# Performance work log

Hardware: AMD Instinct MI355X
Metric: run time of the kernel (lower is better)

The kernel has to match this reference:

```python
import jax, jax.numpy as jnp
import numpy as np


def _conv1d(x, w, pad):
    # torch F.conv1d is cross-correlation; so is lax.conv_general_dilated.
    # x: (k, c_in, N), w: (c_out, c_in, K) -> (k, c_out, N + 2*pad - K + 1)
    return jax.lax.conv_general_dilated(
        x, w, window_strides=(1,), padding=[(pad, pad)],
        dimension_numbers=("NCH", "OIH", "NCH"))


def setup_inputs() -> dict:
    key = jax.random.key(0)
    k1, k2, k3, k4, k5 = jax.random.split(key, 5)
    k_b, c_out, c_in, N, m = 4, 64, 8, 4096, 8
    z_real = jax.random.normal(k1, (k_b, c_in, N), dtype=jnp.float32)
    z_imag = jax.random.normal(k2, (k_b, c_in, N), dtype=jnp.float32)
    A = jax.random.uniform(k3, (c_out, c_in, 1), jnp.float32, 0.75, 1.25)
    beta = jax.random.uniform(k4, (c_out, c_in, 1), jnp.float32, -np.pi, np.pi)
    bias = jax.random.uniform(k5, (c_out, 1), jnp.float32, -0.1, 0.1)
    return {"z_real": z_real, "z_imag": z_imag, "A": A, "beta": beta,
            "bias": bias, "m": m}


def reference(z_real, z_imag, A, beta, bias, m):
    k_b, c_in, N = z_real.shape
    am = abs(int(m))
    ker = N // (2 * am)  # self.ker_size

    # Complex harmonic kernel: |A| * exp(i*(beta + 2*pi*m*phi/N))
    phi = jnp.arange(ker, dtype=jnp.float32)
    ang = beta + (2.0 * jnp.pi * m / N) * phi  # (c_out, c_in, ker)
    absA = jnp.abs(A)
    wr = absA * jnp.cos(ang)
    wi = absA * jnp.sin(ang)

    # Complex conv via 4 real convs: (zr + i zi) * (wr + i wi)
    rr = _conv1d(z_real, wr, ker)
    ii = _conv1d(z_imag, wi, ker)
    ri = _conv1d(z_real, wi, ker)
    ir = _conv1d(z_imag, wr, ker)
    zraw_r = rr - ii  # (k, c_out, N + ker + 1)
    zraw_i = ri + ir

    # Aliasing fold: gather shifted copies, mask out-of-range, alternate sign.
    n = jnp.arange(-2 * am + 1, 2 * am + 1, dtype=jnp.int32)  # (4|m|,)
    mu = jnp.arange(N, dtype=jnp.int32)[:, None]              # (N, 1)
    ind = mu + ker * n                                        # (N, 4|m|)
    cond = ((ind > 0) & (ind < N + ker)).astype(jnp.float32)
    ind = jnp.clip(ind, 0, N + ker)
    menos_1 = (-1.0) ** (1.0 + n.astype(jnp.float32))         # alternating sign
    sign = cond * menos_1                                     # (N, 4|m|)

    gr = zraw_r[:, :, ind]  # (k, c_out, N, 4|m|)
    gi = zraw_i[:, :, ind]
    sr = jnp.einsum("kcnm,nm->kcn", gr, sign)
    si = jnp.einsum("kcnm,nm->kcn", gi, sign)

    # activation: sigmoid(|z| + bias) * z / (|z| + 1e-5)
    mag = jnp.sqrt(sr * sr + si * si)
    gate = jax.nn.sigmoid(mag + bias) / (mag + 1e-5)
    return gate * sr, gate * si
```

## Files before the change

### kernel.cpp

```cpp
#include <hip/hip_runtime.h>
#include <math.h>


#define KB   4
#define COUT 64
#define CIN  8
#define NN   4096
#define INV_N   (1.0f / 4096.0f)
#define INV_2PI 0.15915494309189535f

__global__ __launch_bounds__(256) void capa_fused_kernel(
    const float* __restrict__ zr,
    const float* __restrict__ zi,
    const float* __restrict__ A,
    const float* __restrict__ beta,
    const float* __restrict__ bias,
    const int*   __restrict__ m_ptr,
    float* __restrict__ out) {

    const int blk = blockIdx.x;
    const int b = blk >> 6, o = blk & (COUT - 1);
    const int m = *m_ptr;
    const int tid = threadIdx.x;

    float P[CIN], Q[CIN];
    #pragma unroll
    for (int i = 0; i < CIN; ++i) {
        float a  = fabsf(A[o * CIN + i]);
        float rb = beta[o * CIN + i] * INV_2PI;
        P[i] = a * __builtin_amdgcn_cosf(rb);
        Q[i] = a * __builtin_amdgcn_sinf(rb);
    }

    const float4* xr = (const float4*)(zr + b * CIN * NN);
    const float4* xi = (const float4*)(zi + b * CIN * NN);

    float gr = 0.f, hr = 0.f;
    #pragma unroll
    for (int k = 0; k < NN / 4 / 256; ++k) {
        int vidx = tid + k * 256;
        float4 vr[CIN], vi[CIN];
        #pragma unroll
        for (int i = 0; i < CIN; ++i) {
            vr[i] = xr[i * (NN / 4) + vidx];
            vi[i] = xi[i * (NN / 4) + vidx];
        }
        int t0 = vidx * 4;
        #pragma unroll
        for (int j = 0; j < 4; ++j) {
            float X = 0.f, Y = 0.f;
            #pragma unroll
            for (int i = 0; i < CIN; ++i) {
                float a = (&vr[i].x)[j];
                float c2 = (&vi[i].x)[j];
                X += -P[i] * a + Q[i] * c2;
                Y +=  Q[i] * a + P[i] * c2;
            }
            int r = (m * (t0 + j)) & (NN - 1);
            float rev = (float)r * INV_N;
            float s = __builtin_amdgcn_sinf(rev);
            float c = __builtin_amdgcn_cosf(rev);
            gr += c * X + s * Y;
            hr += s * X - c * Y;
        }
    }

    #pragma unroll
    for (int off = 32; off > 0; off >>= 1) {
        gr += __shfl_down(gr, off);
        hr += __shfl_down(hr, off);
    }
    __shared__ float red[4][2];
    int wave = tid >> 6, lane = tid & 63;
    if (lane == 0) { red[wave][0] = gr; red[wave][1] = hr; }
    __syncthreads();
    const float Gr = red[0][0] + red[1][0] + red[2][0] + red[3][0];
    const float Hr = red[0][1] + red[1][1] + red[2][1] + red[3][1];

    const float bo = bias[o];
    float4* out_r = (float4*)(out + ((long)blk << 12));
    float4* out_i = (float4*)(out + (long)KB * COUT * NN + ((long)blk << 12));

    #pragma unroll
    for (int k = 0; k < NN / 4 / 256; ++k) {
        int vidx = tid + k * 256;
        int mu0 = vidx * 4;
        float4 o1, o2;
        #pragma unroll
        for (int j = 0; j < 4; ++j) {
            int r = (m * (mu0 + j)) & (NN - 1);
            float rev = (float)r * INV_N;
            float s = __builtin_amdgcn_sinf(rev);
            float c = __builtin_amdgcn_cosf(rev);
            float sr = -(c * Gr + s * Hr);
            float si = s * Gr - c * Hr;
            float mag = sqrtf(sr * sr + si * si);
            float gate = 1.0f / ((1.0f + __expf(-(mag + bo))) * (mag + 1e-5f));
            (&o1.x)[j] = gate * sr;
            (&o2.x)[j] = gate * si;
        }
        out_r[vidx] = o1;
        out_i[vidx] = o2;
    }
}

extern "C" void kernel_launch(void* const* d_in, const int* in_sizes, int n_in,
                              void* d_out, int out_size, void* d_ws, size_t ws_size,
                              hipStream_t stream) {
    const float* z_real = (const float*)d_in[0];
    const float* z_imag = (const float*)d_in[1];
    const float* A      = (const float*)d_in[2];
    const float* beta   = (const float*)d_in[3];
    const float* bias   = (const float*)d_in[4];
    const int*   m_ptr  = (const int*)d_in[5];
    float* out = (float*)d_out;

    capa_fused_kernel<<<KB * COUT, 256, 0, stream>>>(
        z_real, z_imag, A, beta, bias, m_ptr, out);
}
```

Baseline: 77.98 us.

## Factor input projections into per-channel Fourier partials computed once by separate kernel

The input-dependent inner products against the cos/sin basis are now computed once per (batch, input channel) in a first kernel, split into four chunks and written as partial sums to workspace. A second kernel combines these with the per-output-channel complex weights and produces the gated output. Before, every (batch, output channel) block re-read all input channels and recomputed the same projections, giving 64x redundant loads and FMAs. The cost is an extra kernel launch and a round-trip through global workspace.

```diff
diff --git a/kernel.cpp b/kernel.cpp
--- a/kernel.cpp
+++ b/kernel.cpp
@@ -6,76 +6,92 @@
 #define COUT 64
 #define CIN  8
 #define NN   4096
+#define NCHUNK 4
 #define INV_N   (1.0f / 4096.0f)
 #define INV_2PI 0.15915494309189535f
 
-__global__ __launch_bounds__(256) void capa_fused_kernel(
+__global__ __launch_bounds__(256) void f_partial_kernel(
     const float* __restrict__ zr,
     const float* __restrict__ zi,
+    const int* __restrict__ m_ptr,
+    float* __restrict__ Fp) {
+
+    const int blk = blockIdx.x;
+    const int pair = blk >> 2, chunk = blk & (NCHUNK - 1);
+    const int tid = threadIdx.x;
+    const int m = *m_ptr;
+
+    const float4* xr = (const float4*)(zr + pair * NN) + chunk * 256;
+    const float4* xi = (const float4*)(zi + pair * NN) + chunk * 256;
+    float4 vr = xr[tid];
+    float4 vi = xi[tid];
+
+    const int t0 = (chunk * 256 + tid) * 4;
+    float fcr = 0.f, fsr = 0.f, fci = 0.f, fsi = 0.f;
+    #pragma unroll
+    for (int j = 0; j < 4; ++j) {
+        int r = (m * (t0 + j)) & (NN - 1);
+        float rev = (float)r * INV_N;
+        float s = __builtin_amdgcn_sinf(rev);
+        float c = __builtin_amdgcn_cosf(rev);
+        float a = (&vr.x)[j], b = (&vi.x)[j];
+        fcr += a * c;  fsr += a * s;
+        fci += b * c;  fsi += b * s;
+    }
+    #pragma unroll
+    for (int off = 32; off > 0; off >>= 1) {
+        fcr += __shfl_down(fcr, off);
+        fsr += __shfl_down(fsr, off);
+        fci += __shfl_down(fci, off);
+        fsi += __shfl_down(fsi, off);
+    }
+    __shared__ float red[4][4];
+    int wave = tid >> 6, lane = tid & 63;
+    if (lane == 0) {
+        red[wave][0] = fcr; red[wave][1] = fsr;
+        red[wave][2] = fci; red[wave][3] = fsi;
+    }
+    __syncthreads();
+    if (tid == 0) {
+        Fp[blk * 4 + 0] = red[0][0] + red[1][0] + red[2][0] + red[3][0];
+        Fp[blk * 4 + 1] = red[0][1] + red[1][1] + red[2][1] + red[3][1];
+        Fp[blk * 4 + 2] = red[0][2] + red[1][2] + red[2][2] + red[3][2];
+        Fp[blk * 4 + 3] = red[0][3] + red[1][3] + red[2][3] + red[3][3];
+    }
+}
+
+__global__ __launch_bounds__(256) void out_kernel(
     const float* __restrict__ A,
     const float* __restrict__ beta,
     const float* __restrict__ bias,
-    const int*   __restrict__ m_ptr,
+    const int* __restrict__ m_ptr,
+    const float* __restrict__ Fp,
     float* __restrict__ out) {
 
     const int blk = blockIdx.x;
     const int b = blk >> 6, o = blk & (COUT - 1);
     const int m = *m_ptr;
-    const int tid = threadIdx.x;
 
-    float P[CIN], Q[CIN];
+    float Gr = 0.f, Hr = 0.f;
     #pragma unroll
     for (int i = 0; i < CIN; ++i) {
         float a  = fabsf(A[o * CIN + i]);
         float rb = beta[o * CIN + i] * INV_2PI;
-        P[i] = a * __builtin_amdgcn_cosf(rb);
-        Q[i] = a * __builtin_amdgcn_sinf(rb);
+        float cb = __builtin_amdgcn_cosf(rb);
+        float sb = __builtin_amdgcn_sinf(rb);
+        float P = a * cb, Q = a * sb;
+        const float* f = Fp + (b * CIN + i) * NCHUNK * 4;
+        float Fcr = 0.f, Fsr = 0.f, Fci = 0.f, Fsi = 0.f;
+        #pragma unroll
+        for (int ch = 0; ch < NCHUNK; ++ch) {
+            Fcr += f[ch * 4 + 0];
+            Fsr += f[ch * 4 + 1];
+            Fci += f[ch * 4 + 2];
+            Fsi += f[ch * 4 + 3];
+        }
+        Gr += -P * Fcr + Q * Fsr + Q * Fci + P * Fsi;
+        Hr += -P * Fsr - Q * Fcr + Q * Fsi - P * Fci;
     }
-
-    const float4* xr = (const float4*)(zr + b * CIN * NN);
-    const float4* xi = (const float4*)(zi + b * CIN * NN);
-
-    float gr = 0.f, hr = 0.f;
-    #pragma unroll
-    for (int k = 0; k < NN / 4 / 256; ++k) {
-        int vidx = tid + k * 256;
-        float4 vr[CIN], vi[CIN];
-        #pragma unroll
-        for (int i = 0; i < CIN; ++i) {
-            vr[i] = xr[i * (NN / 4) + vidx];
-            vi[i] = xi[i * (NN / 4) + vidx];
-        }
-        int t0 = vidx * 4;
-        #pragma unroll
-        for (int j = 0; j < 4; ++j) {
-            float X = 0.f, Y = 0.f;
-            #pragma unroll
-            for (int i = 0; i < CIN; ++i) {
-                float a = (&vr[i].x)[j];
-                float c2 = (&vi[i].x)[j];
-                X += -P[i] * a + Q[i] * c2;
-                Y +=  Q[i] * a + P[i] * c2;
-            }
-            int r = (m * (t0 + j)) & (NN - 1);
-            float rev = (float)r * INV_N;
-            float s = __builtin_amdgcn_sinf(rev);
-            float c = __builtin_amdgcn_cosf(rev);
-            gr += c * X + s * Y;
-            hr += s * X - c * Y;
-        }
-    }
-
-    #pragma unroll
-    for (int off = 32; off > 0; off >>= 1) {
-        gr += __shfl_down(gr, off);
-        hr += __shfl_down(hr, off);
-    }
-    __shared__ float red[4][2];
-    int wave = tid >> 6, lane = tid & 63;
-    if (lane == 0) { red[wave][0] = gr; red[wave][1] = hr; }
-    __syncthreads();
-    const float Gr = red[0][0] + red[1][0] + red[2][0] + red[3][0];
-    const float Hr = red[0][1] + red[1][1] + red[2][1] + red[3][1];
 
     const float bo = bias[o];
     float4* out_r = (float4*)(out + ((long)blk << 12));
@@ -83,7 +99,7 @@
 
     #pragma unroll
     for (int k = 0; k < NN / 4 / 256; ++k) {
-        int vidx = tid + k * 256;
+        int vidx = threadIdx.x + k * 256;
         int mu0 = vidx * 4;
         float4 o1, o2;
         #pragma unroll
@@ -114,7 +130,8 @@
     const float* bias   = (const float*)d_in[4];
     const int*   m_ptr  = (const int*)d_in[5];
     float* out = (float*)d_out;
+    float* Fp  = (float*)d_ws;
 
-    capa_fused_kernel<<<KB * COUT, 256, 0, stream>>>(
-        z_real, z_imag, A, beta, bias, m_ptr, out);
+    f_partial_kernel<<<KB * CIN * NCHUNK, 256, 0, stream>>>(z_real, z_imag, m_ptr, Fp);
+    out_kernel<<<KB * COUT, 256, 0, stream>>>(A, beta, bias, m_ptr, Fp, out);
 }
```

Result: faster. 71.59 us (-8.2%).
